# Kernel optimization log

Hardware: AMD Instinct MI355X
Metric: run time of the kernel (lower is better)

The kernel has to match this reference:

```python
import jax, jax.numpy as jnp
import numpy as np

# PennyLane default.gaussian conventions: hbar = 2, means vector in (x, p) per-wire
# quadratures; expval(X(w)) = mu_x[w], expval(P(w)) = mu_p[w].
_SQRT_2HBAR = 2.0  # sqrt(2 * hbar) with hbar = 2


def _run_circuit(x, disp, sq, bs):
    """Evolve Gaussian means for all samples at once.

    x: [B, N] input displacements (phi=0)
    disp, sq: [L, N, 2] (magnitude, phase)
    bs: [L, N-1, 2] (theta-logit, phi)
    Returns (mu_x, mu_p) each [B, N].
    """
    L, N = disp.shape[0], disp.shape[1]
    mx = _SQRT_2HBAR * x          # initial Displacement(x_i, 0) on each wire
    mp = jnp.zeros_like(x)
    for l in range(L):
        # Displacement(a, phi) on every wire (different wires commute)
        a, dphi = disp[l, :, 0], disp[l, :, 1]
        mx = mx + _SQRT_2HBAR * a * jnp.cos(dphi)
        mp = mp + _SQRT_2HBAR * a * jnp.sin(dphi)
        # Squeezing(|r|, phi) symplectic [[ch-cp*sh, -sp*sh], [-sp*sh, ch+cp*sh]]
        r, sphi = jnp.abs(sq[l, :, 0]), sq[l, :, 1]
        ch, sh = jnp.cosh(r), jnp.sinh(r)
        cp, sp = jnp.cos(sphi), jnp.sin(sphi)
        mx, mp = (ch - cp * sh) * mx - sp * sh * mp, -sp * sh * mx + (ch + cp * sh) * mp
        # Beamsplitter(sigmoid(t), phi) on (w, w+1): sequential, overlapping wires
        for w in range(N - 1):
            th = jax.nn.sigmoid(bs[l, w, 0])
            bphi = bs[l, w, 1]
            ct, st = jnp.cos(th), jnp.sin(th)
            cpb, spb = jnp.cos(bphi), jnp.sin(bphi)
            x1, x2 = mx[:, w], mx[:, w + 1]
            p1, p2 = mp[:, w], mp[:, w + 1]
            nx1 = ct * x1 - cpb * st * x2 - spb * st * p2
            nx2 = cpb * st * x1 + ct * x2 - spb * st * p1
            np1 = spb * st * x2 + ct * p1 - cpb * st * p2
            np2 = spb * st * x1 + cpb * st * p1 + ct * p2
            mx = mx.at[:, w].set(nx1).at[:, w + 1].set(nx2)
            mp = mp.at[:, w].set(np1).at[:, w + 1].set(np2)
    return mx, mp


def setup_inputs() -> dict:
    key = jax.random.key(0)
    k1, k2, k3, k4 = jax.random.split(key, 4)
    B, N, L = 1048576, 16, 6
    return {
        "x": jax.random.normal(k1, (B, N), dtype=jnp.float32),
        "displacements": jax.random.normal(k2, (2, L, N, 2), dtype=jnp.float32),
        "squeezing": jax.random.normal(k3, (2, L, N, 2), dtype=jnp.float32),
        "beamsplitter": jax.random.normal(k4, (2, L, N - 1, 2), dtype=jnp.float32),
    }


def reference(x, displacements, squeezing, beamsplitter):
    # Parameter set 0 feeds the X-quadrature circuit, set 1 the P-quadrature circuit.
    mx0, _ = _run_circuit(x, displacements[0], squeezing[0], beamsplitter[0])
    _, mp1 = _run_circuit(x, displacements[1], squeezing[1], beamsplitter[1])
    return jnp.concatenate([mx0, mp1], axis=-1)  # [B, 2N]
```

## Files before the change

kernel.cpp:

```cpp
#include <hip/hip_runtime.h>
#include <math.h>

#define NM 16
#define NL 6
#define NW 15
#define S2H 2.0f
#define BLK 256

typedef float v4f __attribute__((ext_vector_type(4)));


__global__ __launch_bounds__(640) void cv_precompute(
    const float* __restrict__ disp,
    const float* __restrict__ sq,
    const float* __restrict__ bs,
    float* __restrict__ ws)
{
    __shared__ float dxc[2][NL][NM], dpc[2][NL][NM];
    __shared__ float s00[2][NL][NM], s01[2][NL][NM], s11[2][NL][NM];
    __shared__ float bct[2][NL][NW], bcs[2][NL][NW], bss[2][NL][NW];

    int t = threadIdx.x;
    if (t < 192) {
        int c = t / 96, rem = t % 96, l = rem / NM, n = rem % NM;
        float a  = disp[((c*NL + l)*NM + n)*2 + 0];
        float ph = disp[((c*NL + l)*NM + n)*2 + 1];
        dxc[c][l][n] = S2H * a * cosf(ph);
        dpc[c][l][n] = S2H * a * sinf(ph);
    } else if (t < 384) {
        int i = t - 192;
        int c = i / 96, rem = i % 96, l = rem / NM, n = rem % NM;
        float r  = fabsf(sq[((c*NL + l)*NM + n)*2 + 0]);
        float ph = sq[((c*NL + l)*NM + n)*2 + 1];
        float ch = coshf(r), sh = sinhf(r);
        float cp = cosf(ph), sp = sinf(ph);
        s00[c][l][n] = ch - cp*sh;
        s01[c][l][n] = -sp*sh;
        s11[c][l][n] = ch + cp*sh;
    } else if (t < 564) {
        int i = t - 384;
        int c = i / 90, rem = i % 90, l = rem / NW, w = rem % NW;
        float z  = bs[((c*NL + l)*NW + w)*2 + 0];
        float ph = bs[((c*NL + l)*NW + w)*2 + 1];
        float th = 1.0f / (1.0f + expf(-z));
        float ct = cosf(th), st = sinf(th);
        bct[c][l][w] = ct;
        bcs[c][l][w] = cosf(ph) * st;
        bss[c][l][w] = sinf(ph) * st;
    }
    __syncthreads();

    if (t >= 34) return;
    int c = t / 17;
    int col = t % 17;
    bool isBias = (col == NM);

    float mx[NM], mp[NM];
    #pragma unroll
    for (int n = 0; n < NM; ++n) { mx[n] = 0.f; mp[n] = 0.f; }
    if (!isBias) mx[col] = S2H;

    for (int l = 0; l < NL; ++l) {
        if (isBias) {
            #pragma unroll
            for (int n = 0; n < NM; ++n) { mx[n] += dxc[c][l][n]; mp[n] += dpc[c][l][n]; }
        }
        #pragma unroll
        for (int n = 0; n < NM; ++n) {
            float a = s00[c][l][n], b = s01[c][l][n], d = s11[c][l][n];
            float nx  = a*mx[n] + b*mp[n];
            float npp = b*mx[n] + d*mp[n];
            mx[n] = nx; mp[n] = npp;
        }
        #pragma unroll
        for (int w = 0; w < NW; ++w) {
            float ct = bct[c][l][w], cst = bcs[c][l][w], sst = bss[c][l][w];
            float x1 = mx[w], x2 = mx[w+1], p1 = mp[w], p2 = mp[w+1];
            mx[w]   = ct*x1  - cst*x2 - sst*p2;
            mx[w+1] = cst*x1 + ct*x2  - sst*p1;
            mp[w]   = sst*x2 + ct*p1  - cst*p2;
            mp[w+1] = sst*x1 + cst*p1 + ct*p2;
        }
    }

    if (c == 0) {
        if (!isBias) {
            #pragma unroll
            for (int n = 0; n < NM; ++n) ws[n*16 + col] = mx[n];
        } else {
            #pragma unroll
            for (int n = 0; n < NM; ++n) ws[512 + n] = mx[n];
        }
    } else {
        if (!isBias) {
            #pragma unroll
            for (int n = 0; n < NM; ++n) ws[(16 + n)*16 + col] = mp[n];
        } else {
            #pragma unroll
            for (int n = 0; n < NM; ++n) ws[512 + 16 + n] = mp[n];
        }
    }
}

__global__ __launch_bounds__(256, 4) void cv_apply(
    const float* __restrict__ x,
    const float* __restrict__ ws,
    float* __restrict__ out,
    long long B)
{
    __shared__ float4 st[BLK * 8];

    const int t = threadIdx.x;
    const long long b0 = (long long)blockIdx.x * BLK;
    const long long b = b0 + t;
    const bool live = (b < B);

    float xr[16];
    if (live) {
        const float4* xp = (const float4*)(x + b * 16);
        #pragma unroll
        for (int q = 0; q < 4; ++q) {
            float4 v = xp[q];
            xr[q*4+0] = v.x; xr[q*4+1] = v.y;
            xr[q*4+2] = v.z; xr[q*4+3] = v.w;
        }
    } else {
        #pragma unroll
        for (int e = 0; e < 16; ++e) xr[e] = 0.f;
    }

    float acc[32];
    #pragma unroll
    for (int n = 0; n < 32; ++n) {
        float a = ws[512 + n];
        #pragma unroll
        for (int e = 0; e < 16; ++e)
            a = fmaf(ws[n * 16 + e], xr[e], a);
        acc[n] = a;
    }

    #pragma unroll
    for (int j = 0; j < 8; ++j) {
        float4 v = make_float4(acc[j*4+0], acc[j*4+1], acc[j*4+2], acc[j*4+3]);
        st[t * 8 + (j ^ (t & 7))] = v;
    }
    __syncthreads();

    v4f* __restrict__ op = (v4f*)(out + b0 * 32);
    const long long umax = (B - b0) * 8;
    #pragma unroll
    for (int i = 0; i < 8; ++i) {
        int u = i * BLK + t;
        if (u < umax) {
            int s = u >> 3, j = u & 7;
            float4 v = st[s * 8 + (j ^ (s & 7))];
            v4f r; r[0] = v.x; r[1] = v.y; r[2] = v.z; r[3] = v.w;
            __builtin_nontemporal_store(r, op + u);
        }
    }
}

extern "C" void kernel_launch(void* const* d_in, const int* in_sizes, int n_in,
                              void* d_out, int out_size, void* d_ws, size_t ws_size,
                              hipStream_t stream) {
    const float* x    = (const float*)d_in[0];
    const float* disp = (const float*)d_in[1];
    const float* sq   = (const float*)d_in[2];
    const float* bs   = (const float*)d_in[3];
    float* ws  = (float*)d_ws;
    float* out = (float*)d_out;

    long long B = in_sizes[0] / NM;

    cv_precompute<<<1, 640, 0, stream>>>(disp, sq, bs, ws);

    int blocks = (int)((B + BLK - 1) / BLK);
    cv_apply<<<blocks, BLK, 0, stream>>>(x, ws, out, B);
}
```

Before: 51.96 us.

## Compute affine map with bf16 MFMA 32x32x16 instead of scalar FMAs

The precompute kernel now writes the 32x16 affine matrix in bf16, laid out as MFMA B-fragments, and keeps the bias in fp32. The apply kernel converts each x row to bf16 and runs one mfma_f32_32x32x16_bf16 per wave for 32 rows, then restages the result through shared memory for coalesced nontemporal stores. This swaps the 512 scalar FMAs per row for a matrix instruction and reloads the block at 128 rows. Rounding both inputs and weights to bf16 reduces accuracy and may exceed tolerance, since some coefficients can be large after cosh/sinh squeezing. The kernel is likely memory bound, so the compute savings may matter little.

```diff
diff --git a/kernel.cpp b/kernel.cpp
--- a/kernel.cpp
+++ b/kernel.cpp
@@ -5,10 +5,17 @@
 #define NL 6
 #define NW 15
 #define S2H 2.0f
-#define BLK 256
 
 typedef float v4f __attribute__((ext_vector_type(4)));
+typedef short bf16x8 __attribute__((ext_vector_type(8)));
+typedef float f32x16 __attribute__((ext_vector_type(16)));
 
+
+__device__ __forceinline__ unsigned short f2bf(float f) {
+    union { float f; unsigned int u; } v; v.f = f;
+    unsigned int r = (v.u + 0x7fffu + ((v.u >> 16) & 1u)) >> 16;
+    return (unsigned short)r;
+}
 
 __global__ __launch_bounds__(640) void cv_precompute(
     const float* __restrict__ disp,
@@ -83,78 +90,76 @@
         }
     }
 
-    if (c == 0) {
-        if (!isBias) {
-            #pragma unroll
-            for (int n = 0; n < NM; ++n) ws[n*16 + col] = mx[n];
-        } else {
-            #pragma unroll
-            for (int n = 0; n < NM; ++n) ws[512 + n] = mx[n];
+    ushort* bfp  = (ushort*)ws;
+    float* biasp = ws + 256;
+    if (!isBias) {
+        #pragma unroll
+        for (int n = 0; n < NM; ++n) {
+            int row = 16*c + n;
+            float val = (c == 0) ? mx[n] : mp[n];
+            int lane = row + 32 * (col >> 3);
+            int slot = col & 7;
+            bfp[lane * 8 + slot] = f2bf(val);
         }
     } else {
-        if (!isBias) {
-            #pragma unroll
-            for (int n = 0; n < NM; ++n) ws[(16 + n)*16 + col] = mp[n];
-        } else {
-            #pragma unroll
-            for (int n = 0; n < NM; ++n) ws[512 + 16 + n] = mp[n];
-        }
+        #pragma unroll
+        for (int n = 0; n < NM; ++n)
+            biasp[16*c + n] = (c == 0) ? mx[n] : mp[n];
     }
 }
 
-__global__ __launch_bounds__(256, 4) void cv_apply(
+__global__ __launch_bounds__(256) void cv_apply(
     const float* __restrict__ x,
     const float* __restrict__ ws,
     float* __restrict__ out,
     long long B)
 {
-    __shared__ float4 st[BLK * 8];
+    __shared__ float st[128 * 32];
+    const int t = threadIdx.x;
+    const int lane = t & 63;
+    const int wave = t >> 6;
+    const int n = lane & 31;
+    const int kg = lane >> 5;
 
-    const int t = threadIdx.x;
-    const long long b0 = (long long)blockIdx.x * BLK;
-    const long long b = b0 + t;
-    const bool live = (b < B);
+    const bf16x8 bfrag = *(const bf16x8*)((const ushort*)ws + lane * 8);
+    const float  bn    = (ws + 256)[n];
 
-    float xr[16];
-    if (live) {
-        const float4* xp = (const float4*)(x + b * 16);
-        #pragma unroll
-        for (int q = 0; q < 4; ++q) {
-            float4 v = xp[q];
-            xr[q*4+0] = v.x; xr[q*4+1] = v.y;
-            xr[q*4+2] = v.z; xr[q*4+3] = v.w;
-        }
+    const long long b0 = (long long)blockIdx.x * 128;
+    const long long row = b0 + wave * 32 + n;
+
+    float xv[8];
+    if (row < B) {
+        const float4* xp = (const float4*)(x + row * 16 + kg * 8);
+        float4 v0 = xp[0], v1 = xp[1];
+        xv[0]=v0.x; xv[1]=v0.y; xv[2]=v0.z; xv[3]=v0.w;
+        xv[4]=v1.x; xv[5]=v1.y; xv[6]=v1.z; xv[7]=v1.w;
     } else {
         #pragma unroll
-        for (int e = 0; e < 16; ++e) xr[e] = 0.f;
+        for (int j = 0; j < 8; ++j) xv[j] = 0.f;
     }
+    bf16x8 afrag;
+    #pragma unroll
+    for (int j = 0; j < 8; ++j) afrag[j] = (short)f2bf(xv[j]);
 
-    float acc[32];
-    #pragma unroll
-    for (int n = 0; n < 32; ++n) {
-        float a = ws[512 + n];
-        #pragma unroll
-        for (int e = 0; e < 16; ++e)
-            a = fmaf(ws[n * 16 + e], xr[e], a);
-        acc[n] = a;
-    }
+    f32x16 acc = {};
+    acc = __builtin_amdgcn_mfma_f32_32x32x16_bf16(afrag, bfrag, acc, 0, 0, 0);
 
     #pragma unroll
-    for (int j = 0; j < 8; ++j) {
-        float4 v = make_float4(acc[j*4+0], acc[j*4+1], acc[j*4+2], acc[j*4+3]);
-        st[t * 8 + (j ^ (t & 7))] = v;
+    for (int r = 0; r < 16; ++r) {
+        int m = (r & 3) + 8 * (r >> 2) + 4 * kg;
+        st[(wave * 32 + m) * 32 + n] = acc[r] + bn;
     }
     __syncthreads();
 
     v4f* __restrict__ op = (v4f*)(out + b0 * 32);
-    const long long umax = (B - b0) * 8;
+    const long long u4max = (B - b0 < 128 ? B - b0 : 128) * 8;
+    const float4* stv = (const float4*)st;
     #pragma unroll
-    for (int i = 0; i < 8; ++i) {
-        int u = i * BLK + t;
-        if (u < umax) {
-            int s = u >> 3, j = u & 7;
-            float4 v = st[s * 8 + (j ^ (s & 7))];
-            v4f r; r[0] = v.x; r[1] = v.y; r[2] = v.z; r[3] = v.w;
+    for (int i = 0; i < 4; ++i) {
+        int u = i * 256 + t;
+        if (u < u4max) {
+            float4 v = stv[u];
+            v4f r; r[0]=v.x; r[1]=v.y; r[2]=v.z; r[3]=v.w;
             __builtin_nontemporal_store(r, op + u);
         }
     }
@@ -174,6 +179,6 @@
 
     cv_precompute<<<1, 640, 0, stream>>>(disp, sq, bs, ws);
 
-    int blocks = (int)((B + BLK - 1) / BLK);
-    cv_apply<<<blocks, BLK, 0, stream>>>(x, ws, out, B);
+    int blocks = (int)((B + 127) / 128);
+    cv_apply<<<blocks, 256, 0, stream>>>(x, ws, out, B);
 }
```

Result: faster. 44.68 us (-14.0%).
